# Optimization experiments

Hardware: AMD Instinct MI355X
Metric: run time of the kernel (lower is better)

## Reference

```python
import jax, jax.numpy as jnp
import numpy as np

EMB, HID, VOC, NLAYERS, TLEN = 256, 512, 32000, 2, 64
SRC_LEN, BS = 128, 64
DEC_HID = 2 * HID  # decoder hidden = hidden_dim * 2


def _p(key, shape, scale=0.05):
    return jax.random.normal(key, shape, dtype=jnp.float32) * scale


def setup_inputs() -> dict:
    key = jax.random.key(0)
    ks = jax.random.split(key, 24)
    d = {}
    d["sentences"] = jax.random.randint(ks[0], (SRC_LEN, BS), 0, VOC)
    d["targets"] = jax.random.randint(ks[1], (TLEN, BS), 0, VOC)
    d["emb"] = _p(ks[2], (VOC, EMB))
    # encoder: bidirectional, 2 layers; gate order i,f,g,o (PyTorch)
    d["enc0_Wih"] = _p(ks[3], (2, 4 * HID, EMB))
    d["enc0_Whh"] = _p(ks[4], (2, 4 * HID, HID))
    d["enc0_bih"] = _p(ks[5], (2, 4 * HID))
    d["enc0_bhh"] = _p(ks[6], (2, 4 * HID))
    d["enc1_Wih"] = _p(ks[7], (2, 4 * HID, 2 * HID))
    d["enc1_Whh"] = _p(ks[8], (2, 4 * HID, HID))
    d["enc1_bih"] = _p(ks[9], (2, 4 * HID))
    d["enc1_bhh"] = _p(ks[10], (2, 4 * HID))
    # decoder: unidirectional, 2 layers, hidden DEC_HID
    d["dec0_Wih"] = _p(ks[11], (4 * DEC_HID, EMB))
    d["dec0_Whh"] = _p(ks[12], (4 * DEC_HID, DEC_HID))
    d["dec0_bih"] = _p(ks[13], (4 * DEC_HID,))
    d["dec0_bhh"] = _p(ks[14], (4 * DEC_HID,))
    d["dec1_Wih"] = _p(ks[15], (4 * DEC_HID, DEC_HID))
    d["dec1_Whh"] = _p(ks[16], (4 * DEC_HID, DEC_HID))
    d["dec1_bih"] = _p(ks[17], (4 * DEC_HID,))
    d["dec1_bhh"] = _p(ks[18], (4 * DEC_HID,))
    d["W_out"] = _p(ks[19], (VOC, DEC_HID))
    d["b_out"] = _p(ks[20], (VOC,))
    return d


def lstm_scan(x, h0, c0, Wih, Whh, bih, bhh, reverse=False):
    # x: (T,B,In). Precompute input projection for the whole sequence.
    xw = jnp.einsum('tbi,gi->tbg', x, Wih) + bih  # (T,B,4H)

    def step(carry, g_in):
        h, c = carry
        g = g_in + h @ Whh.T + bhh
        i, f, gg, o = jnp.split(g, 4, axis=-1)
        c = jax.nn.sigmoid(f) * c + jax.nn.sigmoid(i) * jnp.tanh(gg)
        h = jax.nn.sigmoid(o) * jnp.tanh(c)
        return (h, c), h

    (hT, cT), ys = jax.lax.scan(step, (h0, c0), xw, reverse=reverse)
    return ys, hT, cT


def _forward(sentences, targets, emb,
             enc0_Wih, enc0_Whh, enc0_bih, enc0_bhh,
             enc1_Wih, enc1_Whh, enc1_bih, enc1_bhh,
             dec0_Wih, dec0_Whh, dec0_bih, dec0_bhh,
             dec1_Wih, dec1_Whh, dec1_bih, dec1_bhh,
             W_out, b_out):
    bs = sentences.shape[1]
    x = emb[sentences]  # (S,B,E)
    z = jnp.zeros((bs, HID), jnp.float32)
    enc_layers = ((enc0_Wih, enc0_Whh, enc0_bih, enc0_bhh),
                  (enc1_Wih, enc1_Whh, enc1_bih, enc1_bhh))
    hs, cs = [], []
    for Wih, Whh, bih, bhh in enc_layers:
        yf, hf, cf = lstm_scan(x, z, z, Wih[0], Whh[0], bih[0], bhh[0])
        yb, hb, cb = lstm_scan(x, z, z, Wih[1], Whh[1], bih[1], bhh[1], reverse=True)
        x = jnp.concatenate([yf, yb], axis=-1)  # (S,B,2H)
        hs.append(jnp.concatenate([hf, hb], axis=-1))  # _reshape_hidden concat
        cs.append(jnp.concatenate([cf, cb], axis=-1))
    # teacher forcing: decoder inputs are last source token, then targets[:-1]
    dec_tokens = jnp.concatenate([sentences[-1:], targets[:-1]], axis=0)  # (T,B)
    y = emb[dec_tokens]  # (T,B,E); dropout is identity in eval mode
    dec_layers = ((dec0_Wih, dec0_Whh, dec0_bih, dec0_bhh),
                  (dec1_Wih, dec1_Whh, dec1_bih, dec1_bhh))
    for l, (Wih, Whh, bih, bhh) in enumerate(dec_layers):
        y, _, _ = lstm_scan(y, hs[l], cs[l], Wih, Whh, bih, bhh)
    logits = jnp.einsum('tbh,vh->tbv', y, W_out) + b_out  # (T,B,V)
    return jax.nn.log_softmax(logits, axis=-1)


def reference(sentences, targets, emb,
              enc0_Wih, enc0_Whh, enc0_bih, enc0_bhh,
              enc1_Wih, enc1_Whh, enc1_bih, enc1_bhh,
              dec0_Wih, dec0_Whh, dec0_bih, dec0_bhh,
              dec1_Wih, dec1_Whh, dec1_bih, dec1_bhh,
              W_out, b_out):
    return _forward(sentences, targets, emb,
                    enc0_Wih, enc0_Whh, enc0_bih, enc0_bhh,
                    enc1_Wih, enc1_Whh, enc1_bih, enc1_bhh,
                    dec0_Wih, dec0_Whh, dec0_bih, dec0_bhh,
                    dec1_Wih, dec1_Whh, dec1_bih, dec1_bhh,
                    W_out, b_out)
```

## Files before the change

kernel.cpp:

```cpp
#include <hip/hip_runtime.h>

#define S_LEN 128
#define T_LEN 64
#define BSZ   64
#define EMBD  256
#define HID_  512
#define DHID_ 1024
#define VOC_  32000
#define HSTR  1024

typedef float  f4_t  __attribute__((ext_vector_type(4)));
typedef float  f32x4 __attribute__((ext_vector_type(4)));
typedef short  s16x8 __attribute__((ext_vector_type(8)));
typedef __bf16 bf16x8 __attribute__((ext_vector_type(8)));
typedef unsigned short u16x4 __attribute__((ext_vector_type(4)));
typedef int    i32x2 __attribute__((ext_vector_type(2)));

#define WS_CS   0ull
#define WS_BAR  (WS_CS + 131072ull)
#define WS_BF   (WS_BAR + 32768ull)
#define U_X0B   0ull
#define U_HE0   (U_X0B  + 2097152ull)
#define U_HE1   (U_HE0  + 8388608ull)
#define U_HD0   (U_HE1  + 8388608ull)
#define U_HD1   (U_HD0  + 4194304ull)
#define U_HSB   (U_HD1  + 4194304ull)
#define U_E0W   (U_HSB  + 131072ull)
#define U_E1W   (U_E0W  + 1048576ull)
#define U_D0W   (U_E1W  + 4194304ull)
#define U_D1W   (U_D0W  + 1048576ull)
#define U_XWA   (U_D1W  + 4194304ull)
#define U_XWB   (U_XWA  + 16777216ull)
#define U_WOUT  (U_XWB  + 16777216ull)

__device__ __forceinline__ unsigned short f2bf(float x) {
    unsigned u = __builtin_bit_cast(unsigned, x);
    return (unsigned short)((u + 0x7fffu + ((u >> 16) & 1u)) >> 16);
}
__device__ __forceinline__ float bf2f(unsigned u) {
    return __builtin_bit_cast(float, u << 16);
}

__device__ __forceinline__ f4_t sc_load4(const void* p) {
    f4_t v;
    asm volatile("global_load_dwordx4 %0, %1, off sc0 sc1" : "=v"(v) : "v"(p));
    return v;
}
__device__ __forceinline__ int sc_load1(const int* p) {
    int v;
    asm volatile("global_load_dword %0, %1, off sc0 sc1\n\ts_waitcnt vmcnt(0)"
                 : "=v"(v) : "v"(p) : "memory");
    return v;
}
__device__ __forceinline__ void sc_store_int(int* p, int v) {
    asm volatile("global_store_dword %0, %1, off sc0 sc1" :: "v"(p), "v"(v) : "memory");
}
__device__ __forceinline__ void sc_store_short(unsigned short* p, unsigned v) {
    asm volatile("global_store_short %0, %1, off sc0 sc1" :: "v"(p), "v"(v) : "memory");
}
__device__ __forceinline__ i32x2 g_load8(const void* p) {
    i32x2 v;
    asm volatile("global_load_dwordx2 %0, %1, off" : "=v"(v) : "v"(p));
    return v;
}
__device__ __forceinline__ void wait_vm0() {
    asm volatile("s_waitcnt vmcnt(0)" ::: "memory");
}
__device__ __forceinline__ void wait_vm8() {
    asm volatile("s_waitcnt vmcnt(8)" ::: "memory");
}

__device__ __forceinline__ void gload_lds16(const void* g, void* l) {
    __builtin_amdgcn_global_load_lds(
        (const __attribute__((address_space(1))) void*)g,
        (__attribute__((address_space(3))) void*)l, 16, 0, 0);
}

__device__ __forceinline__ float sigmoidf_(float x) { return 1.f / (1.f + expf(-x)); }

__global__ __launch_bounds__(256) void f2b_kernel(
    const float* __restrict__ in, unsigned short* __restrict__ out, int n4)
{
    const int stride = gridDim.x * 256;
    for (int i = blockIdx.x * 256 + threadIdx.x; i < n4; i += stride) {
        const float4 v = reinterpret_cast<const float4*>(in)[i];
        u16x4 o = { f2bf(v.x), f2bf(v.y), f2bf(v.z), f2bf(v.w) };
        reinterpret_cast<u16x4*>(out)[i] = o;
    }
}

__global__ __launch_bounds__(64) void embed_src_kernel(
    const int* __restrict__ toks, const float* __restrict__ emb,
    unsigned short* __restrict__ out)
{
    const int i = blockIdx.x;
    const int tok = toks[i];
    const float4 v = reinterpret_cast<const float4*>(emb + (size_t)tok * EMBD)[threadIdx.x];
    u16x4 o = { f2bf(v.x), f2bf(v.y), f2bf(v.z), f2bf(v.w) };
    reinterpret_cast<u16x4*>(out + (size_t)i * EMBD)[threadIdx.x] = o;
}

__global__ __launch_bounds__(64) void embed_dec_kernel(
    const int* __restrict__ sent, const int* __restrict__ targ,
    const float* __restrict__ emb, unsigned short* __restrict__ out)
{
    const int i = blockIdx.x;
    const int t = i >> 6, b = i & 63;
    const int tok = (t == 0) ? sent[(S_LEN - 1) * BSZ + b] : targ[(t - 1) * BSZ + b];
    const float4 v = reinterpret_cast<const float4*>(emb + (size_t)tok * EMBD)[threadIdx.x];
    u16x4 o = { f2bf(v.x), f2bf(v.y), f2bf(v.z), f2bf(v.w) };
    reinterpret_cast<u16x4*>(out + (size_t)i * EMBD)[threadIdx.x] = o;
}

__global__ __launch_bounds__(256) void gemm_bf16_kernel(
    const unsigned short* __restrict__ A, const unsigned short* __restrict__ B,
    const float* __restrict__ b1, const float* __restrict__ b2,
    void* __restrict__ Cv, int M, int N, int K, int nTN, int tmode)
{
    __shared__ __align__(16) unsigned short As[128 * 64];
    __shared__ __align__(16) unsigned short Bs[128 * 64];

    const int tid  = threadIdx.x;
    const int lane = tid & 63;
    const int wv   = tid >> 6;
    const int wm   = wv >> 1, wn = wv & 1;

    const int nwg = gridDim.x;
    const int q = nwg >> 3, r = nwg & 7;
    const int xcd = blockIdx.x & 7, io = blockIdx.x >> 3;
    const int wg = (xcd < r ? xcd * (q + 1) : r * (q + 1) + (xcd - r) * q) + io;
    const int bm = (wg / nTN) * 128;
    const int bn = (wg % nTN) * 128;

    f32x4 acc[4][4];
#pragma unroll
    for (int i = 0; i < 4; ++i)
#pragma unroll
        for (int j = 0; j < 4; ++j) acc[i][j] = (f32x4)0.f;

    const int lin_base = wv * 1024 + lane * 16;

    for (int k0 = 0; k0 < K; k0 += 64) {
        __syncthreads();
#pragma unroll
        for (int qc = 0; qc < 4; ++qc) {
            const int lin = qc * 4096 + lin_base;
            const int row = lin >> 7;
            const int c   = (lin >> 4) & 7;
            const int sc  = c ^ (row & 7);
            const size_t gofs  = (size_t)(bm + row) * K + k0 + sc * 8;
            const size_t gofsB = (size_t)(bn + row) * K + k0 + sc * 8;
            char* ldst  = (char*)As + qc * 4096 + wv * 1024;
            char* ldstB = (char*)Bs + qc * 4096 + wv * 1024;
            gload_lds16(A + gofs, ldst);
            gload_lds16(B + gofsB, ldstB);
        }
        asm volatile("s_waitcnt vmcnt(0)" ::: "memory");
        __syncthreads();
#pragma unroll
        for (int ks = 0; ks < 2; ++ks) {
            bf16x8 af[4], bfv[4];
            const int ca = ks * 4 + (lane >> 4);
#pragma unroll
            for (int f = 0; f < 4; ++f) {
                const int ra = wm * 64 + f * 16 + (lane & 15);
                af[f] = __builtin_bit_cast(bf16x8,
                    *(const s16x8*)((const char*)As + ra * 128 + ((ca ^ (ra & 7)) << 4)));
                const int rb = wn * 64 + f * 16 + (lane & 15);
                bfv[f] = __builtin_bit_cast(bf16x8,
                    *(const s16x8*)((const char*)Bs + rb * 128 + ((ca ^ (rb & 7)) << 4)));
            }
#pragma unroll
            for (int i = 0; i < 4; ++i)
#pragma unroll
                for (int j = 0; j < 4; ++j)
                    acc[i][j] = __builtin_amdgcn_mfma_f32_16x16x32_bf16(
                        af[i], bfv[j], acc[i][j], 0, 0, 0);
        }
    }

    const int col0 = bn + wn * 64 + (lane & 15);
    if (tmode == 0) {
        float* C = (float*)Cv;
        const int row0 = bm + wm * 64 + ((lane >> 4) << 2);
#pragma unroll
        for (int i = 0; i < 4; ++i) {
#pragma unroll
            for (int j = 0; j < 4; ++j) {
                const int col = col0 + j * 16;
                float bias = b1[col];
                if (b2) bias += b2[col];
#pragma unroll
                for (int rg = 0; rg < 4; ++rg)
                    C[(size_t)(row0 + i * 16 + rg) * N + col] = acc[i][j][rg] + bias;
            }
        }
    } else {
        unsigned short* C = (unsigned short*)Cv;
        const int tblk = (bm >> 6) + wm;
        const int rb = (lane >> 4) << 2;
#pragma unroll
        for (int i = 0; i < 4; ++i) {
#pragma unroll
            for (int j = 0; j < 4; ++j) {
                const int col = col0 + j * 16;
                float bias = b1[col];
                if (b2) bias += b2[col];
                u16x4 o = { f2bf(acc[i][j][0] + bias), f2bf(acc[i][j][1] + bias),
                            f2bf(acc[i][j][2] + bias), f2bf(acc[i][j][3] + bias) };
                *reinterpret_cast<u16x4*>(&C[((size_t)tblk * N + col) * 64 + rb + i * 16]) = o;
            }
        }
    }
}

template<int H_T>
__global__ __launch_bounds__(256, 1) void lstm_mfma_scan(
    const unsigned short* __restrict__ xw0, const unsigned short* __restrict__ xw1,
    const float* __restrict__ Whh0, const float* __restrict__ Whh1,
    const unsigned short* __restrict__ h0b, const float* __restrict__ c0,
    unsigned short* __restrict__ hist,
    unsigned short* __restrict__ hsb, float* __restrict__ csd,
    int T, int ndir, int rev_mask, int* bar)
{
    constexpr int KST = H_T / 32;
    constexpr int CH  = H_T / 8;
    constexpr int CPT = CH / 8;
    constexpr int NBH = CPT / 8;
    constexpr int NCB = H_T / 8;

    __shared__ __align__(16) unsigned short h_lds[32 * H_T];
    __shared__ __align__(16) unsigned short w_lds[32 * H_T];

    const int tid  = threadIdx.x;
    const int lane = tid & 63;
    const int w    = tid >> 6;
    const int bq   = w & 1;
    const int rh   = w >> 1;
    const int n    = lane & 15;
    const int kg   = lane >> 4;
    const int g    = n >> 2;
    const int cell = rh * 4 + (n & 3);

    const int nbpd = 2 * NCB;
    const int dir  = blockIdx.x / nbpd;
    const int rem  = blockIdx.x - dir * nbpd;
    const int bg   = rem / NCB;
    const int cb   = rem - bg * NCB;
    const int m0c  = cb * 8;
    const int rev  = (rev_mask >> dir) & 1;
    const unsigned short* xw = dir ? xw1 : xw0;
    const float* Whh = dir ? Whh1 : Whh0;
    const int dcol = dir * H_T;
    const int b0   = bg * 32;

    int* myflag = bar + blockIdx.x * 32;
    const int* pollflag = bar +
        ((dir * nbpd + bg * NCB) + (tid < NCB ? tid : 0)) * 32;
    const bool polls = (tid < NCB);

    for (int idx = tid; idx < 32 * CH; idx += 256) {
        const int r_  = idx / CH, cc_ = idx - r_ * CH;
        const int gg_ = r_ >> 3, cl_ = r_ & 7;
        const float* wp = Whh + (size_t)(gg_ * H_T + m0c + cl_) * H_T + cc_ * 8;
        const float4 lo = *reinterpret_cast<const float4*>(wp);
        const float4 hi = *reinterpret_cast<const float4*>(wp + 4);
        s16x8 rr;
        rr[0] = (short)f2bf(lo.x); rr[1] = (short)f2bf(lo.y);
        rr[2] = (short)f2bf(lo.z); rr[3] = (short)f2bf(lo.w);
        rr[4] = (short)f2bf(hi.x); rr[5] = (short)f2bf(hi.y);
        rr[6] = (short)f2bf(hi.z); rr[7] = (short)f2bf(hi.w);
        *(s16x8*)((char*)w_lds + r_ * (2 * H_T) + ((cc_ ^ (r_ & 7)) << 4)) = rr;
    }

    float cst[4] = {0.f, 0.f, 0.f, 0.f};
    if (g == 0 && c0) {
#pragma unroll
        for (int rg = 0; rg < 4; ++rg)
            cst[rg] = c0[(size_t)(b0 + bq * 16 + kg * 4 + rg) * HSTR + dcol + m0c + cell];
    }
    float hnv[4];

    const unsigned short* xbase =
        xw + ((size_t)(g * H_T + m0c + cell)) * 64 + b0 + bq * 16 + kg * 4;
    i32x2 xg;
    auto issue_xg = [&](int ttn) {
        xg = g_load8(xbase + (size_t)ttn * (4 * H_T) * 64);
    };

    const int rW  = g * 8 + cell;
    const int rWx = rW & 7;
    const int rA  = bq * 16 + n;
    const int rAx = rA & 7;

    issue_xg(rev ? (T - 1) : 0);
    __syncthreads();

    for (int s = 0; s < T; ++s) {
        const int tt = rev ? (T - 1 - s) : s;

        if (s > 0) {
            int ok = polls ? 0 : 1;
            for (;;) {
                if (!ok) ok = (sc_load1(pollflag) >= s) ? 1 : 0;
                if (__syncthreads_and(ok)) break;
            }
        }

        const unsigned short* hb;
        size_t tofs;
        if (s == 0) { hb = h0b; tofs = 0; }
        else {
            const int tp = rev ? (tt + 1) : (tt - 1);
            hb = hist; tofs = (size_t)tp * (64 * 1024);
        }

        f32x4 acc = {0.f, 0.f, 0.f, 0.f};
        if (hb) {
            f4_t buf[2][8];
            auto issue = [&](int bt) {
#pragma unroll
                for (int jj = 0; jj < 8; ++jj) {
                    const int idx = (bt * 8 + jj) * 256 + tid;
                    const int rr_ = idx / CH, cc_ = idx - (idx / CH) * CH;
                    buf[bt & 1][jj] = sc_load4(
                        hb + tofs + (size_t)(b0 + rr_) * 1024 + dcol + cc_ * 8);
                }
            };
            auto writeb = [&](int bt) {
#pragma unroll
                for (int jj = 0; jj < 8; ++jj) {
                    const int idx = (bt * 8 + jj) * 256 + tid;
                    const int rr_ = idx / CH, cc_ = idx - (idx / CH) * CH;
                    *(f4_t*)((char*)h_lds + rr_ * (2 * H_T) + ((cc_ ^ (rr_ & 7)) << 4))
                        = buf[bt & 1][jj];
                }
            };
            if (NBH == 1) {
                issue(0); wait_vm0(); writeb(0);
            } else {
                issue(0); issue(1);
                wait_vm8(); writeb(0);
                wait_vm0(); writeb(1);
            }
            __syncthreads();

#pragma unroll
            for (int ks = 0; ks < KST; ++ks) {
                const int ca = ks * 4 + kg;
                const bf16x8 a = __builtin_bit_cast(bf16x8,
                    *(const s16x8*)((const char*)h_lds + rA * (2 * H_T) + ((ca ^ rAx) << 4)));
                const bf16x8 bfr = __builtin_bit_cast(bf16x8,
                    *(const s16x8*)((const char*)w_lds + rW * (2 * H_T) + ((ca ^ rWx) << 4)));
                acc = __builtin_amdgcn_mfma_f32_16x16x32_bf16(a, bfr, acc, 0, 0, 0);
            }
        }

        asm volatile("s_waitcnt vmcnt(0)" : "+v"(xg) :: "memory");
        const unsigned x0u = (unsigned)xg[0], x1u = (unsigned)xg[1];
        float xwf[4] = { bf2f(x0u & 0xffffu), bf2f(x0u >> 16),
                         bf2f(x1u & 0xffffu), bf2f(x1u >> 16) };

        const bool is2 = (g == 2);
        const float kk = is2 ? 2.f : 1.f;
        const float sub = is2 ? 1.f : 0.f;
        float act[4];
#pragma unroll
        for (int rg = 0; rg < 4; ++rg) {
            const float p = acc[rg] + xwf[rg];
            act[rg] = kk * sigmoidf_(kk * p) - sub;
        }
        float x8[4], x4a[4], x4b[4];
#pragma unroll
        for (int rg = 0; rg < 4; ++rg) {
            x8[rg]  = __shfl_xor(act[rg], 8);
            x4a[rg] = __shfl_xor(act[rg], 4);
            x4b[rg] = __shfl_xor(x8[rg], 4);
        }
        if (g == 0) {
#pragma unroll
            for (int rg = 0; rg < 4; ++rg) {
                cst[rg] = x4a[rg] * cst[rg] + act[rg] * x8[rg];
                hnv[rg] = x4b[rg] * tanhf(cst[rg]);
                sc_store_short(hist + (size_t)tt * (64 * 1024)
                               + (size_t)(b0 + bq * 16 + kg * 4 + rg) * 1024
                               + dcol + m0c + cell, (unsigned)f2bf(hnv[rg]));
            }
        }
        wait_vm0();
        __syncthreads();
        if (s + 1 < T) {
            if (tid == 0) sc_store_int(myflag, s + 1);
            issue_xg(rev ? (T - 2 - s) : (s + 1));
        }
    }

    if (hsb && g == 0) {
#pragma unroll
        for (int rg = 0; rg < 4; ++rg) {
            const int b_ = b0 + bq * 16 + kg * 4 + rg;
            hsb[(size_t)b_ * 1024 + dcol + m0c + cell] = f2bf(hnv[rg]);
            csd[(size_t)b_ * HSTR + dcol + m0c + cell] = cst[rg];
        }
    }
}

__global__ __launch_bounds__(256) void logsoftmax_kernel(float* __restrict__ x, int n4)
{
    const int tid = threadIdx.x;
    float4* p = reinterpret_cast<float4*>(x + (size_t)blockIdx.x * (n4 * 4));
    float m = -3.0e38f, s = 0.f;
    for (int cc = tid; cc < n4; cc += 256) {
        const float4 v = p[cc];
        const float vv[4] = { v.x, v.y, v.z, v.w };
#pragma unroll
        for (int e = 0; e < 4; ++e) {
            const float z = vv[e];
            if (z > m) { s = s * expf(m - z) + 1.f; m = z; }
            else       { s += expf(z - m); }
        }
    }
    __shared__ float ms[256], ss[256];
    ms[tid] = m; ss[tid] = s;
    __syncthreads();
    for (int off = 128; off > 0; off >>= 1) {
        if (tid < off) {
            const float m2 = ms[tid + off], s2 = ss[tid + off];
            const float m1 = ms[tid],       s1 = ss[tid];
            const float M = fmaxf(m1, m2);
            ss[tid] = s1 * expf(m1 - M) + s2 * expf(m2 - M);
            ms[tid] = M;
        }
        __syncthreads();
    }
    const float ML = ms[0] + logf(ss[0]);
    for (int cc = tid; cc < n4; cc += 256) {
        float4 v = p[cc];
        v.x -= ML; v.y -= ML; v.z -= ML; v.w -= ML;
        p[cc] = v;
    }
}

extern "C" void kernel_launch(void* const* d_in, const int* in_sizes, int n_in,
                              void* d_out, int out_size, void* d_ws, size_t ws_size,
                              hipStream_t stream)
{
    const int*   sent  = (const int*)d_in[0];
    const int*   targ  = (const int*)d_in[1];
    const float* emb   = (const float*)d_in[2];
    const float* e0Wih = (const float*)d_in[3];
    const float* e0Whh = (const float*)d_in[4];
    const float* e0bih = (const float*)d_in[5];
    const float* e0bhh = (const float*)d_in[6];
    const float* e1Wih = (const float*)d_in[7];
    const float* e1Whh = (const float*)d_in[8];
    const float* e1bih = (const float*)d_in[9];
    const float* e1bhh = (const float*)d_in[10];
    const float* d0Wih = (const float*)d_in[11];
    const float* d0Whh = (const float*)d_in[12];
    const float* d0bih = (const float*)d_in[13];
    const float* d0bhh = (const float*)d_in[14];
    const float* d1Wih = (const float*)d_in[15];
    const float* d1Whh = (const float*)d_in[16];
    const float* d1bih = (const float*)d_in[17];
    const float* d1bhh = (const float*)d_in[18];
    const float* Wout  = (const float*)d_in[19];
    const float* bout  = (const float*)d_in[20];

    float* ws  = (float*)d_ws;
    float* cs  = ws + WS_CS;
    int*   bar = (int*)(ws + WS_BAR);
    unsigned short* ub    = (unsigned short*)(ws + WS_BF);
    unsigned short* x0b   = ub + U_X0B;
    unsigned short* h_e0  = ub + U_HE0;
    unsigned short* h_e1  = ub + U_HE1;
    unsigned short* h_d0  = ub + U_HD0;
    unsigned short* h_d1  = ub + U_HD1;
    unsigned short* hsb   = ub + U_HSB;
    unsigned short* e0Wb  = ub + U_E0W;
    unsigned short* e1Wb  = ub + U_E1W;
    unsigned short* d0Wb  = ub + U_D0W;
    unsigned short* d1Wb  = ub + U_D1W;
    unsigned short* xwA   = ub + U_XWA;
    unsigned short* xwB   = ub + U_XWB;
    unsigned short* Woutb = ub + U_WOUT;
    float* out = (float*)d_out;

    hipMemsetAsync(bar, 0, 4 * 8192 * sizeof(int), stream);

    f2b_kernel<<<256, 256, 0, stream>>>(e0Wih, e0Wb, 1048576 / 4);
    f2b_kernel<<<512, 256, 0, stream>>>(e1Wih, e1Wb, 4194304 / 4);
    f2b_kernel<<<256, 256, 0, stream>>>(d0Wih, d0Wb, 1048576 / 4);
    f2b_kernel<<<512, 256, 0, stream>>>(d1Wih, d1Wb, 4194304 / 4);
    f2b_kernel<<<2048, 256, 0, stream>>>(Wout, Woutb, (VOC_ * DHID_) / 4);

    embed_src_kernel<<<S_LEN * BSZ, 64, 0, stream>>>(sent, emb, x0b);
    gemm_bf16_kernel<<<64 * 16, 256, 0, stream>>>(x0b, e0Wb, e0bih, e0bhh, xwA,
                                                  S_LEN * BSZ, 2048, EMBD, 16, 1);
    gemm_bf16_kernel<<<64 * 16, 256, 0, stream>>>(x0b, e0Wb + 2048ull * 256,
                                                  e0bih + 2048, e0bhh + 2048, xwB,
                                                  S_LEN * BSZ, 2048, EMBD, 16, 1);
    lstm_mfma_scan<512><<<256, 256, 0, stream>>>(xwA, xwB, e0Whh, e0Whh + 2048ull * 512,
                                                 nullptr, nullptr, h_e0,
                                                 hsb, cs, S_LEN, 2, 2, bar);
    gemm_bf16_kernel<<<64 * 16, 256, 0, stream>>>(h_e0, e1Wb, e1bih, e1bhh, xwA,
                                                  S_LEN * BSZ, 2048, 2 * HID_, 16, 1);
    gemm_bf16_kernel<<<64 * 16, 256, 0, stream>>>(h_e0, e1Wb + 2048ull * 1024,
                                                  e1bih + 2048, e1bhh + 2048, xwB,
                                                  S_LEN * BSZ, 2048, 2 * HID_, 16, 1);
    lstm_mfma_scan<512><<<256, 256, 0, stream>>>(xwA, xwB, e1Whh, e1Whh + 2048ull * 512,
                                                 nullptr, nullptr, h_e1,
                                                 hsb + 65536, cs + 65536,
                                                 S_LEN, 2, 2, bar + 8192);
    embed_dec_kernel<<<T_LEN * BSZ, 64, 0, stream>>>(sent, targ, emb, x0b);
    gemm_bf16_kernel<<<32 * 32, 256, 0, stream>>>(x0b, d0Wb, d0bih, d0bhh, xwA,
                                                  T_LEN * BSZ, 4 * DHID_, EMBD, 32, 1);
    lstm_mfma_scan<1024><<<256, 256, 0, stream>>>(xwA, nullptr, d0Whh, nullptr,
                                                  hsb, cs, h_d0,
                                                  nullptr, nullptr, T_LEN, 1, 0,
                                                  bar + 2 * 8192);
    gemm_bf16_kernel<<<32 * 32, 256, 0, stream>>>(h_d0, d1Wb, d1bih, d1bhh, xwB,
                                                  T_LEN * BSZ, 4 * DHID_, DHID_, 32, 1);
    lstm_mfma_scan<1024><<<256, 256, 0, stream>>>(xwB, nullptr, d1Whh, nullptr,
                                                  hsb + 65536, cs + 65536, h_d1,
                                                  nullptr, nullptr, T_LEN, 1, 0,
                                                  bar + 3 * 8192);
    gemm_bf16_kernel<<<32 * 250, 256, 0, stream>>>(h_d1, Woutb, bout, nullptr, out,
                                                   T_LEN * BSZ, VOC_, DHID_, 250, 0);
    logsoftmax_kernel<<<T_LEN * BSZ, 256, 0, stream>>>(out, VOC_ / 4);
}
```

Baseline: 3.031 ms.

## Restructure LSTM scan into per-wave batch slices with wave-level flag polling

Reworks the recurrent LSTM scan so each block owns 4 hidden cells across all 64 batch rows, with each wave handling its own 16-row batch slice. Each wave now loads its own h slice into a private LDS region, runs its own MFMA chain, and publishes and polls per-wave flags. This removes the block-wide __syncthreads barriers from the recurrence step. The intent is to cut cross-block synchronization latency on the serial recurrence, at the cost of more flags to poll per wave (NF loads per lane), a larger barrier area, and each wave reloading the full hidden row for its batch slice.

New measurement: 4.067 ms. 1.34x slower.

```diff
diff --git a/kernel.cpp b/kernel.cpp
--- a/kernel.cpp
+++ b/kernel.cpp
@@ -18,7 +18,7 @@
 
 #define WS_CS   0ull
 #define WS_BAR  (WS_CS + 131072ull)
-#define WS_BF   (WS_BAR + 32768ull)
+#define WS_BF   (WS_BAR + 65536ull)
 #define U_X0B   0ull
 #define U_HE0   (U_X0B  + 2097152ull)
 #define U_HE1   (U_HE0  + 8388608ull)
@@ -46,10 +46,9 @@
     asm volatile("global_load_dwordx4 %0, %1, off sc0 sc1" : "=v"(v) : "v"(p));
     return v;
 }
-__device__ __forceinline__ int sc_load1(const int* p) {
+__device__ __forceinline__ int sc_load1_nw(const int* p) {
     int v;
-    asm volatile("global_load_dword %0, %1, off sc0 sc1\n\ts_waitcnt vmcnt(0)"
-                 : "=v"(v) : "v"(p) : "memory");
+    asm volatile("global_load_dword %0, %1, off sc0 sc1" : "=v"(v) : "v"(p));
     return v;
 }
 __device__ __forceinline__ void sc_store_int(int* p, int v) {
@@ -66,8 +65,8 @@
 __device__ __forceinline__ void wait_vm0() {
     asm volatile("s_waitcnt vmcnt(0)" ::: "memory");
 }
-__device__ __forceinline__ void wait_vm8() {
-    asm volatile("s_waitcnt vmcnt(8)" ::: "memory");
+__device__ __forceinline__ void wait_vm16() {
+    asm volatile("s_waitcnt vmcnt(16)" ::: "memory");
 }
 
 __device__ __forceinline__ void gload_lds16(const void* g, void* l) {
@@ -215,7 +214,7 @@
 }
 
 template<int H_T>
-__global__ __launch_bounds__(256, 1) void lstm_mfma_scan(
+__global__ __launch_bounds__(256, 1) void lstm_wave_scan(
     const unsigned short* __restrict__ xw0, const unsigned short* __restrict__ xw1,
     const float* __restrict__ Whh0, const float* __restrict__ Whh1,
     const unsigned short* __restrict__ h0b, const float* __restrict__ c0,
@@ -223,46 +222,39 @@
     unsigned short* __restrict__ hsb, float* __restrict__ csd,
     int T, int ndir, int rev_mask, int* bar)
 {
-    constexpr int KST = H_T / 32;
+    constexpr int NCB = H_T / 4;
+    constexpr int NF  = NCB / 64;
+    constexpr int NCH = H_T / 512;
     constexpr int CH  = H_T / 8;
-    constexpr int CPT = CH / 8;
-    constexpr int NBH = CPT / 8;
-    constexpr int NCB = H_T / 8;
-
-    __shared__ __align__(16) unsigned short h_lds[32 * H_T];
-    __shared__ __align__(16) unsigned short w_lds[32 * H_T];
+
+    __shared__ __align__(16) unsigned short w_lds[16 * H_T];
+    __shared__ __align__(16) unsigned short h_lds[4][16 * 512];
 
     const int tid  = threadIdx.x;
     const int lane = tid & 63;
     const int w    = tid >> 6;
-    const int bq   = w & 1;
-    const int rh   = w >> 1;
     const int n    = lane & 15;
     const int kg   = lane >> 4;
     const int g    = n >> 2;
-    const int cell = rh * 4 + (n & 3);
-
-    const int nbpd = 2 * NCB;
-    const int dir  = blockIdx.x / nbpd;
-    const int rem  = blockIdx.x - dir * nbpd;
-    const int bg   = rem / NCB;
-    const int cb   = rem - bg * NCB;
-    const int m0c  = cb * 8;
+    const int cl   = n & 3;
+    const int dir  = blockIdx.x / NCB;
+    const int blk  = blockIdx.x - dir * NCB;
+    const int m0   = blk * 4;
     const int rev  = (rev_mask >> dir) & 1;
     const unsigned short* xw = dir ? xw1 : xw0;
     const float* Whh = dir ? Whh1 : Whh0;
     const int dcol = dir * H_T;
-    const int b0   = bg * 32;
-
-    int* myflag = bar + blockIdx.x * 32;
-    const int* pollflag = bar +
-        ((dir * nbpd + bg * NCB) + (tid < NCB ? tid : 0)) * 32;
-    const bool polls = (tid < NCB);
-
-    for (int idx = tid; idx < 32 * CH; idx += 256) {
-        const int r_  = idx / CH, cc_ = idx - r_ * CH;
-        const int gg_ = r_ >> 3, cl_ = r_ & 7;
-        const float* wp = Whh + (size_t)(gg_ * H_T + m0c + cl_) * H_T + cc_ * 8;
+    const int b0   = w * 16;
+
+    int* myflag = bar + (((dir * NCB + blk) << 2) + w) * 16;
+    const int* pf[NF];
+#pragma unroll
+    for (int j = 0; j < NF; ++j)
+        pf[j] = bar + (((dir * NCB + (lane + j * 64)) << 2) + w) * 16;
+
+    for (int idx = tid; idx < 16 * CH; idx += 256) {
+        const int r_ = idx / CH, cc = idx - r_ * CH;
+        const float* wp = Whh + (size_t)((r_ >> 2) * H_T + m0 + (r_ & 3)) * H_T + cc * 8;
         const float4 lo = *reinterpret_cast<const float4*>(wp);
         const float4 hi = *reinterpret_cast<const float4*>(wp + 4);
         s16x8 rr;
@@ -270,29 +262,23 @@
         rr[2] = (short)f2bf(lo.z); rr[3] = (short)f2bf(lo.w);
         rr[4] = (short)f2bf(hi.x); rr[5] = (short)f2bf(hi.y);
         rr[6] = (short)f2bf(hi.z); rr[7] = (short)f2bf(hi.w);
-        *(s16x8*)((char*)w_lds + r_ * (2 * H_T) + ((cc_ ^ (r_ & 7)) << 4)) = rr;
+        *(s16x8*)((char*)w_lds + r_ * (2 * H_T) + (((cc & ~7) | ((cc ^ r_) & 7)) << 4)) = rr;
     }
 
     float cst[4] = {0.f, 0.f, 0.f, 0.f};
     if (g == 0 && c0) {
 #pragma unroll
         for (int rg = 0; rg < 4; ++rg)
-            cst[rg] = c0[(size_t)(b0 + bq * 16 + kg * 4 + rg) * HSTR + dcol + m0c + cell];
-    }
-    float hnv[4];
+            cst[rg] = c0[(size_t)(b0 + kg * 4 + rg) * HSTR + dcol + m0 + n];
+    }
+    float hnv[4] = {0.f, 0.f, 0.f, 0.f};
 
     const unsigned short* xbase =
-        xw + ((size_t)(g * H_T + m0c + cell)) * 64 + b0 + bq * 16 + kg * 4;
+        xw + ((size_t)(g * H_T + m0 + cl)) * 64 + b0 + kg * 4;
     i32x2 xg;
     auto issue_xg = [&](int ttn) {
         xg = g_load8(xbase + (size_t)ttn * (4 * H_T) * 64);
     };
-
-    const int rW  = g * 8 + cell;
-    const int rWx = rW & 7;
-    const int rA  = bq * 16 + n;
-    const int rAx = rA & 7;
-
     issue_xg(rev ? (T - 1) : 0);
     __syncthreads();
 
@@ -300,10 +286,16 @@
         const int tt = rev ? (T - 1 - s) : s;
 
         if (s > 0) {
-            int ok = polls ? 0 : 1;
             for (;;) {
-                if (!ok) ok = (sc_load1(pollflag) >= s) ? 1 : 0;
-                if (__syncthreads_and(ok)) break;
+                int f[NF];
+#pragma unroll
+                for (int j = 0; j < NF; ++j) f[j] = sc_load1_nw(pf[j]);
+                wait_vm0();
+                bool ok = true;
+#pragma unroll
+                for (int j = 0; j < NF; ++j) ok &= (f[j] >= s);
+                if (__all(ok)) break;
+                __builtin_amdgcn_s_sleep(4);
             }
         }
 
@@ -317,49 +309,57 @@
 
         f32x4 acc = {0.f, 0.f, 0.f, 0.f};
         if (hb) {
-            f4_t buf[2][8];
-            auto issue = [&](int bt) {
-#pragma unroll
-                for (int jj = 0; jj < 8; ++jj) {
-                    const int idx = (bt * 8 + jj) * 256 + tid;
-                    const int rr_ = idx / CH, cc_ = idx - (idx / CH) * CH;
-                    buf[bt & 1][jj] = sc_load4(
-                        hb + tofs + (size_t)(b0 + rr_) * 1024 + dcol + cc_ * 8);
-                }
-            };
-            auto writeb = [&](int bt) {
-#pragma unroll
-                for (int jj = 0; jj < 8; ++jj) {
-                    const int idx = (bt * 8 + jj) * 256 + tid;
-                    const int rr_ = idx / CH, cc_ = idx - (idx / CH) * CH;
-                    *(f4_t*)((char*)h_lds + rr_ * (2 * H_T) + ((cc_ ^ (rr_ & 7)) << 4))
-                        = buf[bt & 1][jj];
-                }
-            };
-            if (NBH == 1) {
-                issue(0); wait_vm0(); writeb(0);
+            const unsigned short* src = hb + tofs + dcol;
+            char* hl = (char*)&h_lds[w][0];
+            f4_t bufA[16];
+#pragma unroll
+            for (int jj = 0; jj < 16; ++jj)
+                bufA[jj] = sc_load4(src + (size_t)(b0 + jj) * 1024 + lane * 8);
+            f4_t bufB[16];
+            if constexpr (NCH == 2) {
+#pragma unroll
+                for (int jj = 0; jj < 16; ++jj)
+                    bufB[jj] = sc_load4(src + (size_t)(b0 + jj) * 1024 + 512 + lane * 8);
+                wait_vm16();
             } else {
-                issue(0); issue(1);
-                wait_vm8(); writeb(0);
-                wait_vm0(); writeb(1);
-            }
-            __syncthreads();
-
-#pragma unroll
-            for (int ks = 0; ks < KST; ++ks) {
+                wait_vm0();
+            }
+#pragma unroll
+            for (int jj = 0; jj < 16; ++jj)
+                *(f4_t*)(hl + jj * 1024 + (((lane & 56) | ((lane ^ jj) & 7)) << 4)) = bufA[jj];
+#pragma unroll
+            for (int ks = 0; ks < 16; ++ks) {
                 const int ca = ks * 4 + kg;
                 const bf16x8 a = __builtin_bit_cast(bf16x8,
-                    *(const s16x8*)((const char*)h_lds + rA * (2 * H_T) + ((ca ^ rAx) << 4)));
-                const bf16x8 bfr = __builtin_bit_cast(bf16x8,
-                    *(const s16x8*)((const char*)w_lds + rW * (2 * H_T) + ((ca ^ rWx) << 4)));
-                acc = __builtin_amdgcn_mfma_f32_16x16x32_bf16(a, bfr, acc, 0, 0, 0);
+                    *(const s16x8*)(hl + n * 1024 + (((ca & 56) | ((ca ^ n) & 7)) << 4)));
+                const bf16x8 b = __builtin_bit_cast(bf16x8,
+                    *(const s16x8*)((const char*)w_lds + n * (2 * H_T)
+                                    + (((ca & ~7) | ((ca ^ n) & 7)) << 4)));
+                acc = __builtin_amdgcn_mfma_f32_16x16x32_bf16(a, b, acc, 0, 0, 0);
+            }
+            if constexpr (NCH == 2) {
+                wait_vm0();
+#pragma unroll
+                for (int jj = 0; jj < 16; ++jj)
+                    *(f4_t*)(hl + jj * 1024 + (((lane & 56) | ((lane ^ jj) & 7)) << 4)) = bufB[jj];
+#pragma unroll
+                for (int ks = 0; ks < 16; ++ks) {
+                    const int ca = ks * 4 + kg;
+                    const int gc = 64 + ca;
+                    const bf16x8 a = __builtin_bit_cast(bf16x8,
+                        *(const s16x8*)(hl + n * 1024 + (((ca & 56) | ((ca ^ n) & 7)) << 4)));
+                    const bf16x8 b = __builtin_bit_cast(bf16x8,
+                        *(const s16x8*)((const char*)w_lds + n * (2 * H_T)
+                                        + (((gc & ~7) | ((gc ^ n) & 7)) << 4)));
+                    acc = __builtin_amdgcn_mfma_f32_16x16x32_bf16(a, b, acc, 0, 0, 0);
+                }
             }
         }
 
         asm volatile("s_waitcnt vmcnt(0)" : "+v"(xg) :: "memory");
         const unsigned x0u = (unsigned)xg[0], x1u = (unsigned)xg[1];
-        float xwf[4] = { bf2f(x0u & 0xffffu), bf2f(x0u >> 16),
-                         bf2f(x1u & 0xffffu), bf2f(x1u >> 16) };
+        const float xwf[4] = { bf2f(x0u & 0xffffu), bf2f(x0u >> 16),
+                               bf2f(x1u & 0xffffu), bf2f(x1u >> 16) };
 
         const bool is2 = (g == 2);
         const float kk = is2 ? 2.f : 1.f;
@@ -383,14 +383,13 @@
                 cst[rg] = x4a[rg] * cst[rg] + act[rg] * x8[rg];
                 hnv[rg] = x4b[rg] * tanhf(cst[rg]);
                 sc_store_short(hist + (size_t)tt * (64 * 1024)
-                               + (size_t)(b0 + bq * 16 + kg * 4 + rg) * 1024
-                               + dcol + m0c + cell, (unsigned)f2bf(hnv[rg]));
+                               + (size_t)(b0 + kg * 4 + rg) * 1024
+                               + dcol + m0 + n, (unsigned)f2bf(hnv[rg]));
             }
         }
         wait_vm0();
-        __syncthreads();
         if (s + 1 < T) {
-            if (tid == 0) sc_store_int(myflag, s + 1);
+            if (lane == 0) sc_store_int(myflag, s + 1);
             issue_xg(rev ? (T - 2 - s) : (s + 1));
         }
     }
@@ -398,9 +397,9 @@
     if (hsb && g == 0) {
 #pragma unroll
         for (int rg = 0; rg < 4; ++rg) {
-            const int b_ = b0 + bq * 16 + kg * 4 + rg;
-            hsb[(size_t)b_ * 1024 + dcol + m0c + cell] = f2bf(hnv[rg]);
-            csd[(size_t)b_ * HSTR + dcol + m0c + cell] = cst[rg];
+            const int b_ = b0 + kg * 4 + rg;
+            hsb[(size_t)b_ * 1024 + dcol + m0 + n] = f2bf(hnv[rg]);
+            csd[(size_t)b_ * HSTR + dcol + m0 + n] = cst[rg];
         }
     }
 }
@@ -486,7 +485,7 @@
     unsigned short* Woutb = ub + U_WOUT;
     float* out = (float*)d_out;
 
-    hipMemsetAsync(bar, 0, 4 * 8192 * sizeof(int), stream);
+    hipMemsetAsync(bar, 0, 4 * 16384 * sizeof(int), stream);
 
     f2b_kernel<<<256, 256, 0, stream>>>(e0Wih, e0Wb, 1048576 / 4);
     f2b_kernel<<<512, 256, 0, stream>>>(e1Wih, e1Wb, 4194304 / 4);
@@ -500,7 +499,7 @@
     gemm_bf16_kernel<<<64 * 16, 256, 0, stream>>>(x0b, e0Wb + 2048ull * 256,
                                                   e0bih + 2048, e0bhh + 2048, xwB,
                                                   S_LEN * BSZ, 2048, EMBD, 16, 1);
-    lstm_mfma_scan<512><<<256, 256, 0, stream>>>(xwA, xwB, e0Whh, e0Whh + 2048ull * 512,
+    lstm_wave_scan<512><<<256, 256, 0, stream>>>(xwA, xwB, e0Whh, e0Whh + 2048ull * 512,
                                                  nullptr, nullptr, h_e0,
                                                  hsb, cs, S_LEN, 2, 2, bar);
     gemm_bf16_kernel<<<64 * 16, 256, 0, stream>>>(h_e0, e1Wb, e1bih, e1bhh, xwA,
@@ -508,23 +507,23 @@
     gemm_bf16_kernel<<<64 * 16, 256, 0, stream>>>(h_e0, e1Wb + 2048ull * 1024,
                                                   e1bih + 2048, e1bhh + 2048, xwB,
                                                   S_LEN * BSZ, 2048, 2 * HID_, 16, 1);
-    lstm_mfma_scan<512><<<256, 256, 0, stream>>>(xwA, xwB, e1Whh, e1Whh + 2048ull * 512,
+    lstm_wave_scan<512><<<256, 256, 0, stream>>>(xwA, xwB, e1Whh, e1Whh + 2048ull * 512,
                                                  nullptr, nullptr, h_e1,
                                                  hsb + 65536, cs + 65536,
-                                                 S_LEN, 2, 2, bar + 8192);
+                                                 S_LEN, 2, 2, bar + 16384);
     embed_dec_kernel<<<T_LEN * BSZ, 64, 0, stream>>>(sent, targ, emb, x0b);
     gemm_bf16_kernel<<<32 * 32, 256, 0, stream>>>(x0b, d0Wb, d0bih, d0bhh, xwA,
                                                   T_LEN * BSZ, 4 * DHID_, EMBD, 32, 1);
-    lstm_mfma_scan<1024><<<256, 256, 0, stream>>>(xwA, nullptr, d0Whh, nullptr,
+    lstm_wave_scan<1024><<<256, 256, 0, stream>>>(xwA, nullptr, d0Whh, nullptr,
                                                   hsb, cs, h_d0,
                                                   nullptr, nullptr, T_LEN, 1, 0,
-                                                  bar + 2 * 8192);
+                                                  bar + 2 * 16384);
     gemm_bf16_kernel<<<32 * 32, 256, 0, stream>>>(h_d0, d1Wb, d1bih, d1bhh, xwB,
                                                   T_LEN * BSZ, 4 * DHID_, DHID_, 32, 1);
-    lstm_mfma_scan<1024><<<256, 256, 0, stream>>>(xwB, nullptr, d1Whh, nullptr,
+    lstm_wave_scan<1024><<<256, 256, 0, stream>>>(xwB, nullptr, d1Whh, nullptr,
                                                   hsb + 65536, cs + 65536, h_d1,
                                                   nullptr, nullptr, T_LEN, 1, 0,
-                                                  bar + 3 * 8192);
+                                                  bar + 3 * 16384);
     gemm_bf16_kernel<<<32 * 250, 256, 0, stream>>>(h_d1, Woutb, bout, nullptr, out,
                                                    T_LEN * BSZ, VOC_, DHID_, 250, 0);
     logsoftmax_kernel<<<T_LEN * BSZ, 256, 0, stream>>>(out, VOC_ / 4);
```
